# Kernel tuning notes

Hardware: AMD Instinct MI355X
Metric: run time of the kernel (lower is better)

The kernel has to match this reference:

```python
import jax, jax.numpy as jnp
import numpy as np

N = 20000
E = 500000
NS = 128
NT = 128
BN_EPS = 1e-3
DIMS = [NS, 2 * NT, 4 * NT, 2 * NT, NT, NT]


def setup_inputs() -> dict:
    key = jax.random.key(0)
    ks = jax.random.split(key, 32)
    inp = {
        "x": jax.random.normal(ks[0], (N, NS), jnp.float32),
        "edge_index": jax.random.randint(ks[1], (2, E), 0, N),
        "edge_attr": jax.random.uniform(ks[2], (E,), jnp.float32),
    }
    for i in range(5):
        din, dout = DIMS[i], DIMS[i + 1]
        inp[f"W{i+1}"] = jax.random.normal(ks[3 + i], (din, dout), jnp.float32) * (1.0 / np.sqrt(din)).astype(np.float32)
        inp[f"b{i+1}"] = jnp.zeros((dout,), jnp.float32)
    for i in range(4):
        d = DIMS[i + 1]
        inp[f"g{i+1}"] = 1.0 + 0.1 * jax.random.normal(ks[10 + i], (d,), jnp.float32)
        inp[f"be{i+1}"] = 0.1 * jax.random.normal(ks[14 + i], (d,), jnp.float32)
        inp[f"m{i+1}"] = 0.1 * jax.random.normal(ks[18 + i], (d,), jnp.float32)
        inp[f"v{i+1}"] = jax.random.uniform(ks[22 + i], (d,), jnp.float32, minval=0.5, maxval=1.5)
    return inp


def gcn_norm(edge_index, edge_attr, n):
    # PyG gcn_norm with self-loops (fill value 1) and symmetric degree norm.
    loop = jnp.arange(n)
    row = jnp.concatenate([edge_index[0], loop])
    col = jnp.concatenate([edge_index[1], loop])
    w = jnp.concatenate([edge_attr, jnp.ones((n,), edge_attr.dtype)])
    deg = jax.ops.segment_sum(w, col, num_segments=n)
    dinv = jnp.where(deg > 0, jax.lax.rsqrt(deg), 0.0)
    return row, col, dinv[row] * w * dinv[col]


def gcn_conv(h, W, b, row, col, norm, n):
    # out[col] += norm * (h @ W)[row]; then add bias (PyG GCNConv).
    hw = h @ W
    agg = jax.ops.segment_sum(hw[row] * norm[:, None], col, num_segments=n)
    return agg + b


def bn_eval(h, g, be, m, v):
    return (h - m) * jax.lax.rsqrt(v + BN_EPS) * g + be


def reference(x, edge_index, edge_attr,
              W1, b1, W2, b2, W3, b3, W4, b4, W5, b5,
              g1, be1, m1, v1, g2, be2, m2, v2,
              g3, be3, m3, v3, g4, be4, m4, v4):
    n = x.shape[0]
    row, col, norm = gcn_norm(edge_index, edge_attr, n)  # cached=True: shared by all layers
    h = jax.nn.sigmoid(bn_eval(gcn_conv(x, W1, b1, row, col, norm, n), g1, be1, m1, v1))
    h = jax.nn.sigmoid(bn_eval(gcn_conv(h, W2, b2, row, col, norm, n), g2, be2, m2, v2))
    h = jax.nn.sigmoid(bn_eval(gcn_conv(h, W3, b3, row, col, norm, n), g3, be3, m3, v3))
    h = jax.nn.sigmoid(bn_eval(gcn_conv(h, W4, b4, row, col, norm, n), g4, be4, m4, v4))
    h = jax.nn.sigmoid(gcn_conv(h, W5, b5, row, col, norm, n))
    # dropout is identity in eval mode
    x11 = h.T @ h  # [NT, NT]
    x12 = 0.5 * (x11 + x11.T)
    return x12 - jnp.diag(jnp.diag(x12))
```

## Files before the change

kernel.cpp:

```cpp
#include <hip/hip_runtime.h>
#include <hip/hip_bf16.h>
#include <hip/hip_fp8.h>
#include <cstdint>
#include <cstddef>

typedef __hip_bfloat16 bf16;
typedef unsigned char fp8;
typedef __attribute__((ext_vector_type(8))) short short8;
typedef __attribute__((ext_vector_type(4))) float f32x4;
typedef __attribute__((ext_vector_type(2))) float f32x2;

#define NSF 128
#define BN_EPS 1e-3f
#define NR 4
#define SCK 2048


__global__ void passA_kernel(const int* __restrict__ ei, int* __restrict__ fill,
                             int* __restrict__ loc, int E, int n, int rsize) {
    int idx = blockIdx.x * blockDim.x + threadIdx.x;
    if (idx < E) {
        int r = ei[idx];
        int c = ei[E + idx];
        int slot = c * NR + r / rsize;
        loc[idx] = atomicAdd(&fill[slot], 1);
    } else if (idx < E + n) {
        int i = idx - E;
        int slot = i * NR + i / rsize;
        loc[idx] = atomicAdd(&fill[slot], 1);
    }
}


__global__ void scan1_kernel(const int* __restrict__ cnt, int* __restrict__ blksum, int total) {
    __shared__ int red[256];
    int base = blockIdx.x * SCK + threadIdx.x * 8;
    int s = 0;
    #pragma unroll
    for (int i = 0; i < 8; ++i) {
        int idx = base + i;
        if (idx < total) s += cnt[idx];
    }
    red[threadIdx.x] = s;
    __syncthreads();
    for (int off2 = 128; off2 > 0; off2 >>= 1) {
        if (threadIdx.x < off2) red[threadIdx.x] += red[threadIdx.x + off2];
        __syncthreads();
    }
    if (threadIdx.x == 0) blksum[blockIdx.x] = red[0];
}

__global__ void scan2_kernel(int* __restrict__ blksum, int* __restrict__ row_ptr,
                             int nblk, int total) {
    __shared__ int part[256];
    int tid = threadIdx.x;
    int v = (tid < nblk) ? blksum[tid] : 0;
    part[tid] = v;
    __syncthreads();
    for (int off2 = 1; off2 < 256; off2 <<= 1) {
        int t = (tid >= off2) ? part[tid - off2] : 0;
        __syncthreads();
        part[tid] += t;
        __syncthreads();
    }
    if (tid < nblk) blksum[tid] = part[tid] - v;
    if (tid == 255) row_ptr[total] = part[255];
}

__global__ void scan3_kernel(const int* __restrict__ cnt, const int* __restrict__ blkoff,
                             int* __restrict__ row_ptr, int total) {
    __shared__ int part[256];
    int tid = threadIdx.x;
    int base = blockIdx.x * SCK + tid * 8;
    int loc[8]; int s = 0;
    #pragma unroll
    for (int i = 0; i < 8; ++i) {
        int idx = base + i;
        loc[i] = (idx < total) ? cnt[idx] : 0;
        s += loc[i];
    }
    part[tid] = s;
    __syncthreads();
    for (int off2 = 1; off2 < 256; off2 <<= 1) {
        int t = (tid >= off2) ? part[tid - off2] : 0;
        __syncthreads();
        part[tid] += t;
        __syncthreads();
    }
    int run = blkoff[blockIdx.x] + part[tid] - s;
    #pragma unroll
    for (int i = 0; i < 8; ++i) {
        int idx = base + i;
        if (idx < total) { row_ptr[idx] = run; run += loc[i]; }
    }
}

__global__ void passB_kernel(const int* __restrict__ ei, const float* __restrict__ ea,
                             const int* __restrict__ row_ptr, const int* __restrict__ loc,
                             int2* __restrict__ e8, int* __restrict__ csr_col,
                             int E, int n, int rsize) {
    int idx = blockIdx.x * blockDim.x + threadIdx.x;
    if (idx < E) {
        int r = ei[idx];
        int c = ei[E + idx];
        int slot = c * NR + r / rsize;
        int p = row_ptr[slot] + loc[idx];
        int2 rec; rec.x = r; rec.y = __float_as_int(ea[idx]);
        e8[p] = rec;
        csr_col[p] = c;
    } else if (idx < E + n) {
        int i = idx - E;
        int slot = i * NR + i / rsize;
        int p = row_ptr[slot] + loc[idx];
        int2 rec; rec.x = i; rec.y = __float_as_int(1.0f);
        e8[p] = rec;
        csr_col[p] = i;
    }
}

__global__ void degdinv_kernel(const int* __restrict__ row_ptr, const int2* __restrict__ e8,
                               float* __restrict__ dinv, int n) {
    int node = blockIdx.x * blockDim.x + threadIdx.x;
    if (node < n) {
        int s = row_ptr[node * NR], e = row_ptr[(node + 1) * NR];
        float d = 0.0f;
        for (int j = s; j < e; ++j) d += __int_as_float(e8[j].y);
        dinv[node] = (d > 0.0f) ? rsqrtf(d) : 0.0f;
    }
}

__global__ void normw_kernel(const float* __restrict__ dinv, const int* __restrict__ csr_col,
                             int2* __restrict__ e8, int EN) {
    int p = blockIdx.x * blockDim.x + threadIdx.x;
    if (p < EN) {
        int2 rec = e8[p];
        float w = dinv[rec.x] * __int_as_float(rec.y) * dinv[csr_col[p]];
        ((int*)e8)[2 * p + 1] = __float_as_int(w);
    }
}


__device__ inline void store_val(bf16* C, size_t idx, float a) {
    C[idx] = __float2bfloat16(a);
}
__device__ inline void store_val(fp8* C, size_t idx, float a) {
    int packed = __builtin_amdgcn_cvt_pk_fp8_f32(a, a, 0, false);
    C[idx] = (fp8)(packed & 0xff);
}

__global__ void prep_kernel(int* __restrict__ fill, int total,
                            const float* __restrict__ x, fp8* __restrict__ xq, int xcnt,
                            const float* __restrict__ W0, const float* __restrict__ W1,
                            const float* __restrict__ W2, const float* __restrict__ W3,
                            const float* __restrict__ W4,
                            bf16* __restrict__ wtbuf, int wtelems) {
    int idx = blockIdx.x * blockDim.x + threadIdx.x;
    if (idx < total) { fill[idx] = 0; return; }
    idx -= total;
    if (idx < xcnt) {
        store_val(xq, idx, x[idx]);
        return;
    }
    int widx = idx - xcnt;
    if (widx >= wtelems) return;
    const float* W; int K, off;
    if (widx < 32768)       { W = W0; K = 128; off = 0; }
    else if (widx < 163840) { W = W1; K = 256; off = 32768; }
    else if (widx < 294912) { W = W2; K = 512; off = 163840; }
    else if (widx < 327680) { W = W3; K = 256; off = 294912; }
    else                    { W = W4; K = 128; off = 327680; }
    int N2;
    if (widx < 32768) N2 = 256; else if (widx < 163840) N2 = 512;
    else if (widx < 294912) N2 = 256; else N2 = 128;
    int l = widx - off;
    int nn = l / K, kk = l % K;
    wtbuf[widx] = __float2bfloat16(W[(size_t)kk * N2 + nn]);
}


__device__ inline void gl_lds16(const bf16* g, bf16* l) {
    __builtin_amdgcn_global_load_lds(
        (const __attribute__((address_space(1))) void*)g,
        (__attribute__((address_space(3))) void*)l,
        16, 0, 0);
}


template <typename OT>
__global__ __launch_bounds__(256) void mfma_gemm_kernel(
    const bf16* __restrict__ A, const bf16* __restrict__ Wt,
    OT* __restrict__ C, int M, int K, int N, int mode,
    const float* __restrict__ bias, const float* __restrict__ g,
    const float* __restrict__ be, const float* __restrict__ m,
    const float* __restrict__ v) {
    __shared__ bf16 As[64][32];
    __shared__ bf16 Bs[128][32];
    int m0 = blockIdx.x * 64;
    int n0 = blockIdx.y * 128;
    int tid = threadIdx.x;
    int wave = tid >> 6, lane = tid & 63;
    int lrow = lane & 15, quad = lane >> 4;

    f32x4 acc[4][2] = {};

    int srow = lane >> 2;
    int sseg = lane & 3;
    int am = wave * 16 + srow;
    int bn = wave * 32 + srow;
    bool aok = (m0 + am) < M;

    for (int k0 = 0; k0 < K; k0 += 32) {
        if (aok)
            gl_lds16(A + (size_t)(m0 + am) * K + k0 + sseg * 8, &As[am][sseg * 8]);
        gl_lds16(Wt + (size_t)(n0 + bn) * K + k0 + sseg * 8, &Bs[bn][sseg * 8]);
        gl_lds16(Wt + (size_t)(n0 + bn + 16) * K + k0 + sseg * 8, &Bs[bn + 16][sseg * 8]);
        __syncthreads();

        short8 afrag[4], bfrag[2];
        #pragma unroll
        for (int mt = 0; mt < 4; ++mt)
            afrag[mt] = *(const short8*)(&As[mt * 16 + lrow][quad * 8]);
        #pragma unroll
        for (int nt = 0; nt < 2; ++nt)
            bfrag[nt] = *(const short8*)(&Bs[wave * 32 + nt * 16 + lrow][quad * 8]);
        #pragma unroll
        for (int mt = 0; mt < 4; ++mt)
            #pragma unroll
            for (int nt = 0; nt < 2; ++nt)
                acc[mt][nt] = __builtin_amdgcn_mfma_f32_16x16x32_bf16(
                    afrag[mt], bfrag[nt], acc[mt][nt], 0, 0, 0);
        __syncthreads();
    }
    #pragma unroll
    for (int nt = 0; nt < 2; ++nt) {
        int gn = n0 + wave * 32 + nt * 16 + lrow;
        float bsc = 0.0f, scale = 1.0f, mean = 0.0f, beta = 0.0f;
        if (mode == 1) {
            bsc = bias[gn];
            scale = g[gn] * rsqrtf(v[gn] + BN_EPS);
            mean = m[gn];
            beta = be[gn];
        }
        #pragma unroll
        for (int mt = 0; mt < 4; ++mt) {
            #pragma unroll
            for (int rr = 0; rr < 4; ++rr) {
                int gm = m0 + mt * 16 + quad * 4 + rr;
                if (gm < M) {
                    float a = acc[mt][nt][rr];
                    if (mode == 1) {
                        a = (a + bsc - mean) * scale + beta;
                        a = 1.0f / (1.0f + __expf(-a));
                    }
                    store_val(C, (size_t)gm * N + gn, a);
                }
            }
        }
    }
}


template <int VEC> struct F8Vec;
template <> struct F8Vec<2> { typedef unsigned short T; };
template <> struct F8Vec<4> { typedef unsigned int T; };

__device__ inline void fma_f8(unsigned short q, float w, float* acc) {
    f32x2 lo = __builtin_amdgcn_cvt_pk_f32_fp8((unsigned int)q, false);
    acc[0] += w * lo.x;
    acc[1] += w * lo.y;
}
__device__ inline void fma_f8(unsigned int q, float w, float* acc) {
    f32x2 lo = __builtin_amdgcn_cvt_pk_f32_fp8(q, false);
    f32x2 hi = __builtin_amdgcn_cvt_pk_f32_fp8(q, true);
    acc[0] += w * lo.x;
    acc[1] += w * lo.y;
    acc[2] += w * hi.x;
    acc[3] += w * hi.y;
}

template <int VEC>
__global__ __launch_bounds__(256) void agg_fp8_kernel(
    const fp8* __restrict__ hw,
    const int* __restrict__ row_ptr, const int2* __restrict__ e8,
    const float* __restrict__ bias,
    const float* __restrict__ g, const float* __restrict__ be,
    const float* __restrict__ m, const float* __restrict__ v,
    bf16* __restrict__ out, int n, int mode) {
    typedef typename F8Vec<VEC>::T T;
    const int dfeat = VEC * 64;
    int wave = threadIdx.x >> 6;
    int lane = threadIdx.x & 63;
    int node = blockIdx.x * 4 + wave;
    if (node >= n) return;
    int s = row_ptr[node * NR], e = row_ptr[(node + 1) * NR];
    float acc[VEC];
    #pragma unroll
    for (int i = 0; i < VEC; ++i) acc[i] = 0.0f;
    const size_t base = (size_t)lane * VEC;

    int j = s;
    for (; j + 7 < e; j += 8) {
        int2 ew[8];
        #pragma unroll
        for (int u = 0; u < 8; ++u) ew[u] = e8[j + u];
        T q[8];
        #pragma unroll
        for (int u = 0; u < 8; ++u)
            q[u] = *(const T*)(hw + (size_t)ew[u].x * dfeat + base);
        #pragma unroll
        for (int u = 0; u < 8; ++u)
            fma_f8(q[u], __int_as_float(ew[u].y), acc);
    }
    for (; j + 3 < e; j += 4) {
        int2 ew[4];
        #pragma unroll
        for (int u = 0; u < 4; ++u) ew[u] = e8[j + u];
        T q[4];
        #pragma unroll
        for (int u = 0; u < 4; ++u)
            q[u] = *(const T*)(hw + (size_t)ew[u].x * dfeat + base);
        #pragma unroll
        for (int u = 0; u < 4; ++u)
            fma_f8(q[u], __int_as_float(ew[u].y), acc);
    }
    for (; j < e; ++j) {
        int2 ew = e8[j];
        T q = *(const T*)(hw + (size_t)ew.x * dfeat + base);
        fma_f8(q, __int_as_float(ew.y), acc);
    }

    #pragma unroll
    for (int i = 0; i < VEC; ++i) {
        int f = (int)base + i;
        float a = acc[i];
        if (mode != 0) {
            a += bias[f];
            if (mode == 1) {
                float scale = g[f] * rsqrtf(v[f] + BN_EPS);
                a = (a - m[f]) * scale + be[f];
            }
            a = 1.0f / (1.0f + __expf(-a));
        }
        out[(size_t)node * dfeat + f] = __float2bfloat16(a);
    }
}

#define TPAD 8

__global__ __launch_bounds__(256) void htht_mfma_kernel(
    const bf16* __restrict__ h, float* __restrict__ partial, int n) {
    __shared__ bf16 hsT[128][32 + TPAD];
    int b = blockIdx.x;
    int tid = threadIdx.x;
    int wave = tid >> 6, lane = tid & 63;
    int lrow = lane & 15, quad = lane >> 4;

    f32x4 acc[2][8] = {};

    int kk = tid >> 3;
    int seg = tid & 7;

    for (int kt = 0; kt < 8; ++kt) {
        int k0 = b * 256 + kt * 32;
        #pragma unroll
        for (int s2 = 0; s2 < 2; ++s2) {
            int fs = (seg + s2 * 8) * 8;
            int gk = k0 + kk;
            uint4 q; q.x = q.y = q.z = q.w = 0u;
            if (gk < n) q = *(const uint4*)(h + (size_t)gk * 128 + fs);
            const unsigned short* u = (const unsigned short*)&q;
            #pragma unroll
            for (int i = 0; i < 8; ++i)
                *((unsigned short*)&hsT[fs + i][kk]) = u[i];
        }
        __syncthreads();
        short8 af0 = *(const short8*)(&hsT[wave * 32 + lrow][quad * 8]);
        short8 af1 = *(const short8*)(&hsT[wave * 32 + 16 + lrow][quad * 8]);
        #pragma unroll
        for (int t = 0; t < 8; ++t) {
            short8 bfrag = *(const short8*)(&hsT[t * 16 + lrow][quad * 8]);
            acc[0][t] = __builtin_amdgcn_mfma_f32_16x16x32_bf16(af0, bfrag, acc[0][t], 0, 0, 0);
            acc[1][t] = __builtin_amdgcn_mfma_f32_16x16x32_bf16(af1, bfrag, acc[1][t], 0, 0, 0);
        }
        __syncthreads();
    }
    float* p = partial + (size_t)b * 16384;
    #pragma unroll
    for (int a_ = 0; a_ < 2; ++a_) {
        #pragma unroll
        for (int t = 0; t < 8; ++t) {
            #pragma unroll
            for (int rr = 0; rr < 4; ++rr) {
                int gm = wave * 32 + a_ * 16 + quad * 4 + rr;
                int gn = t * 16 + lrow;
                p[gm * 128 + gn] = acc[a_][t][rr];
            }
        }
    }
}

__global__ void reduce_kernel(const float* __restrict__ partial, float* __restrict__ out, int nchunks) {
    int idx = blockIdx.x * blockDim.x + threadIdx.x;
    float s = 0.0f;
    for (int c = 0; c < nchunks; ++c) s += partial[(size_t)c * 16384 + idx];
    int i = idx / 128, j = idx % 128;
    out[idx] = (i == j) ? 0.0f : s;
}

extern "C" void kernel_launch(void* const* d_in, const int* in_sizes, int n_in,
                              void* d_out, int out_size, void* d_ws, size_t ws_size,
                              hipStream_t stream) {
    const float* x  = (const float*)d_in[0];
    const int*   ei = (const int*)d_in[1];
    const float* ea = (const float*)d_in[2];
    const float* W[5];  const float* bvec[5];
    for (int l = 0; l < 5; ++l) { W[l] = (const float*)d_in[3 + 2 * l]; bvec[l] = (const float*)d_in[4 + 2 * l]; }
    const float* g[4]; const float* be[4]; const float* mm[4]; const float* vv[4];
    for (int l = 0; l < 4; ++l) {
        g[l]  = (const float*)d_in[13 + 4 * l];
        be[l] = (const float*)d_in[14 + 4 * l];
        mm[l] = (const float*)d_in[15 + 4 * l];
        vv[l] = (const float*)d_in[16 + 4 * l];
    }
    const int n = in_sizes[0] / NSF;
    const int E = in_sizes[1] / 2;
    const int EN = E + n;
    const int rsize = (n + NR - 1) / NR;
    const int total = n * NR;
    const int nscan = (total + SCK - 1) / SCK;
    const int dims[6] = {128, 256, 512, 256, 128, 128};
    const int wtoff[5] = {0, 32768, 163840, 294912, 327680};
    const int wtelems = 344064;

    auto align = [](size_t o) { return (o + 255) & ~(size_t)255; };
    size_t off = 0;
    float* dinv    = (float*)((char*)d_ws + off); off = align(off + (size_t)n * 4);
    int*   fill    = (int*)  ((char*)d_ws + off); off = align(off + (size_t)total * 4);
    int*   row_ptr = (int*)  ((char*)d_ws + off); off = align(off + ((size_t)total + 1) * 4);
    int*   blksum  = (int*)  ((char*)d_ws + off); off = align(off + (size_t)256 * 4);
    int*   locb    = (int*)  ((char*)d_ws + off); off = align(off + (size_t)EN * 4);
    int2*  e8      = (int2*) ((char*)d_ws + off); off = align(off + (size_t)EN * 8);
    int*   csr_col = (int*)  ((char*)d_ws + off); off = align(off + (size_t)EN * 4);
    bf16*  wtbuf   = (bf16*) ((char*)d_ws + off); off = align(off + (size_t)wtelems * 2);
    fp8*   xq      = (fp8*)  ((char*)d_ws + off); off = align(off + (size_t)n * 128);
    bf16*  hbuf    = (bf16*) ((char*)d_ws + off); off = align(off + (size_t)n * 512 * 2);
    bf16*  abuf    = (bf16*) ((char*)d_ws + off); off = align(off + (size_t)n * 512 * 2);
    fp8*   f8buf   = (fp8*)  ((char*)d_ws + off); off = align(off + (size_t)n * 256);
    const int KCH = (20000 + 255) / 256;
    float* partial = (float*)((char*)d_ws + off); off = align(off + (size_t)KCH * 16384 * 4);

    {
        int xcnt = n * 128;
        int items = total + xcnt + wtelems;
        prep_kernel<<<(items + 255) / 256, 256, 0, stream>>>(fill, total, x, xq, xcnt,
            W[0], W[1], W[2], W[3], W[4], wtbuf, wtelems);
    }

    passA_kernel<<<(EN + 255) / 256, 256, 0, stream>>>(ei, fill, locb, E, n, rsize);
    scan1_kernel<<<nscan, 256, 0, stream>>>(fill, blksum, total);
    scan2_kernel<<<1, 256, 0, stream>>>(blksum, row_ptr, nscan, total);
    scan3_kernel<<<nscan, 256, 0, stream>>>(fill, blksum, row_ptr, total);
    passB_kernel<<<(EN + 255) / 256, 256, 0, stream>>>(ei, ea, row_ptr, locb,
                                                       e8, csr_col, E, n, rsize);
    degdinv_kernel<<<(n + 255) / 256, 256, 0, stream>>>(row_ptr, e8, dinv, n);
    normw_kernel<<<(EN + 255) / 256, 256, 0, stream>>>(dinv, csr_col, e8, EN);

    int ablocks = (n + 3) / 4;
    auto gemm_bf16 = [&](const bf16* A, int l, bf16* C, int mode) {
        int K = dims[l], N = dims[l + 1];
        dim3 gg((n + 63) / 64, N / 128);
        int bi = (l < 4) ? l : 0;
        mfma_gemm_kernel<bf16><<<gg, 256, 0, stream>>>(A, wtbuf + wtoff[l], C, n, K, N, mode,
                                                       bvec[l], g[bi], be[bi], mm[bi], vv[bi]);
    };
    auto gemm_fp8 = [&](const bf16* A, int l, fp8* C, int mode) {
        int K = dims[l], N = dims[l + 1];
        dim3 gg((n + 63) / 64, N / 128);
        int bi = (l < 4) ? l : 0;
        mfma_gemm_kernel<fp8><<<gg, 256, 0, stream>>>(A, wtbuf + wtoff[l], C, n, K, N, mode,
                                                      bvec[l], g[bi], be[bi], mm[bi], vv[bi]);
    };

    agg_fp8_kernel<2><<<ablocks, 256, 0, stream>>>(xq, row_ptr, e8,
        bvec[0], bvec[0], bvec[0], bvec[0], bvec[0], abuf, n, 0);
    gemm_fp8(abuf, 0, f8buf, 1);
    agg_fp8_kernel<4><<<ablocks, 256, 0, stream>>>(f8buf, row_ptr, e8,
        bvec[1], bvec[1], bvec[1], bvec[1], bvec[1], abuf, n, 0);
    gemm_bf16(abuf, 1, hbuf, 1);
    gemm_fp8(hbuf, 2, f8buf, 0);
    agg_fp8_kernel<4><<<ablocks, 256, 0, stream>>>(f8buf, row_ptr, e8,
        bvec[2], g[2], be[2], mm[2], vv[2], abuf, n, 1);
    gemm_fp8(abuf, 3, f8buf, 0);
    agg_fp8_kernel<2><<<ablocks, 256, 0, stream>>>(f8buf, row_ptr, e8,
        bvec[3], g[3], be[3], mm[3], vv[3], hbuf, n, 1);
    gemm_fp8(hbuf, 4, f8buf, 0);
    agg_fp8_kernel<2><<<ablocks, 256, 0, stream>>>(f8buf, row_ptr, e8,
        bvec[4], bvec[4], bvec[4], bvec[4], bvec[4], abuf, n, 2);

    htht_mfma_kernel<<<KCH, 256, 0, stream>>>(abuf, partial, n);
    reduce_kernel<<<16384 / 256, 256, 0, stream>>>(partial, (float*)d_out, KCH);
}
```

Before: 402.4 us.

## Stage edge records in LDS and double-buffer fp8 gathers in aggregation

Each wave now loads up to 64 edge records (source index, weight) at once with one coalesced read into shared memory, then walks them in 16-edge groups. Gathers for the next group of 8 are issued while the previous 8 are being accumulated, keeping more loads in flight. Padding uses zero-weight records that point at node 0, which adds some wasted loads for low-degree nodes. Offsets switch to 32-bit arithmetic, and there is no barrier other than a waitcnt, which relies on each wave only touching its own LDS slice.

```diff
diff --git a/kernel.cpp b/kernel.cpp
--- a/kernel.cpp
+++ b/kernel.cpp
@@ -288,6 +288,7 @@
     bf16* __restrict__ out, int n, int mode) {
     typedef typename F8Vec<VEC>::T T;
     const int dfeat = VEC * 64;
+    __shared__ int2 recs[4][64];
     int wave = threadIdx.x >> 6;
     int lane = threadIdx.x & 63;
     int node = blockIdx.x * 4 + wave;
@@ -296,38 +297,42 @@
     float acc[VEC];
     #pragma unroll
     for (int i = 0; i < VEC; ++i) acc[i] = 0.0f;
-    const size_t base = (size_t)lane * VEC;
-
-    int j = s;
-    for (; j + 7 < e; j += 8) {
-        int2 ew[8];
-        #pragma unroll
-        for (int u = 0; u < 8; ++u) ew[u] = e8[j + u];
-        T q[8];
-        #pragma unroll
-        for (int u = 0; u < 8; ++u)
-            q[u] = *(const T*)(hw + (size_t)ew[u].x * dfeat + base);
-        #pragma unroll
-        for (int u = 0; u < 8; ++u)
-            fma_f8(q[u], __int_as_float(ew[u].y), acc);
-    }
-    for (; j + 3 < e; j += 4) {
-        int2 ew[4];
-        #pragma unroll
-        for (int u = 0; u < 4; ++u) ew[u] = e8[j + u];
-        T q[4];
-        #pragma unroll
-        for (int u = 0; u < 4; ++u)
-            q[u] = *(const T*)(hw + (size_t)ew[u].x * dfeat + base);
-        #pragma unroll
-        for (int u = 0; u < 4; ++u)
-            fma_f8(q[u], __int_as_float(ew[u].y), acc);
-    }
-    for (; j < e; ++j) {
-        int2 ew = e8[j];
-        T q = *(const T*)(hw + (size_t)ew.x * dfeat + base);
-        fma_f8(q, __int_as_float(ew.y), acc);
-    }
+    const unsigned int base = (unsigned int)lane * VEC;
+
+#define LOADG(Q, WV, J0)                                                     \
+    _Pragma("unroll")                                                        \
+    for (int u = 0; u < 8; ++u) {                                            \
+        int2 rec = recs[wave][(J0) + u];                                     \
+        WV[u] = __int_as_float(rec.y);                                       \
+        Q[u] = *(const T*)(hw + ((unsigned int)rec.x * dfeat + base));       \
+    }
+#define CONSUME(Q, WV)                                                       \
+    _Pragma("unroll")                                                        \
+    for (int u = 0; u < 8; ++u) fma_f8(Q[u], WV[u], acc);
+
+    for (int cs = s; cs < e; cs += 64) {
+        int cnt = e - cs; if (cnt > 64) cnt = 64;
+        int2 r0; r0.x = 0; r0.y = 0;
+        if (lane < cnt) r0 = e8[cs + lane];
+        recs[wave][lane] = r0;
+        asm volatile("s_waitcnt vmcnt(0) lgkmcnt(0)" ::: "memory");
+
+        int npad = (cnt + 15) & ~15;
+        T qA[8], qB[8];
+        float wA[8], wB[8];
+        LOADG(qA, wA, 0)
+        LOADG(qB, wB, 8)
+        for (int j0 = 16; j0 < npad; j0 += 16) {
+            CONSUME(qA, wA)
+            LOADG(qA, wA, j0)
+            CONSUME(qB, wB)
+            LOADG(qB, wB, j0 + 8)
+        }
+        CONSUME(qA, wA)
+        CONSUME(qB, wB)
+    }
+#undef LOADG
+#undef CONSUME
 
     #pragma unroll
     for (int i = 0; i < VEC; ++i) {
```

Result: faster. 380.9 us (-5.3%).
